# Kernel optimization log

Measured on AMD Instinct MI355X. Metric: run time of the kernel, lower is better.

Reference implementation:

```python
import jax, jax.numpy as jnp
import numpy as np

D_MODEL = 512; D_STATE = 64; D_CONV = 4; EXPAND = 1; HEADDIM = 128; NGROUPS = 2; CHUNK = 256
D_INNER = EXPAND * (D_MODEL // 2)          # 256
NHEADS = D_INNER // HEADDIM                 # 2
CONV_DIM = D_INNER + 2 * NGROUPS * D_STATE  # 512
D_IN_PROJ = CONV_DIM + NHEADS               # 514

def silu(x):
    return x * jax.nn.sigmoid(x)

def conv1x1(x, w, b):
    # x: (b,c,h,w), w: (o,c)
    return jnp.einsum('bchw,oc->bohw', x, w) + b[None, :, None, None]

def dwconv3x3(x, w, b):
    # depthwise 3x3, SAME padding; w: (c,1,3,3)
    c = x.shape[1]
    y = jax.lax.conv_general_dilated(x, w, (1, 1), 'SAME', feature_group_count=c,
                                     dimension_numbers=('NCHW', 'OIHW', 'NCHW'))
    return y + b[None, :, None, None]

def causal_dwconv1d(x, w, b):
    # x: (b,L,c); w: (c,k). Torch pads k-1 both sides then slices [:L] -> causal left pad.
    k = w.shape[1]
    xp = jnp.pad(x, ((0, 0), (k - 1, 0), (0, 0))).transpose(0, 2, 1)  # (b,c,L+k-1)
    y = jax.lax.conv_general_dilated(xp, w[:, None, :], (1,), 'VALID',
                                     feature_group_count=w.shape[0],
                                     dimension_numbers=('NCH', 'OIH', 'NCH'))
    return y.transpose(0, 2, 1) + b

def axis_attn(x, qw, qb, fw, fb, axis):
    # DualAxisAggAttn single-axis step
    qkv = conv1x1(x, qw, qb)
    c = x.shape[1]
    q, k, v = qkv[:, :1], qkv[:, 1:1 + c], qkv[:, 1 + c:]
    dim = -1 if axis == 'W' else -2
    scores = jax.nn.softmax(q, axis=dim)
    ctx = jnp.sum(k * scores, axis=dim, keepdims=True)
    out = x + jax.nn.sigmoid(v) * ctx
    return conv1x1(out, fw, fb)

def segsum(x):
    # x: (...,T) -> (...,T,T) lower-triangular segment sums, -inf above diagonal
    T = x.shape[-1]
    cs = jnp.cumsum(x, -1)
    d = cs[..., :, None] - cs[..., None, :]
    mask = jnp.tril(jnp.ones((T, T), bool))
    return jnp.where(mask, d, -jnp.inf)

def ssd(X, A, B, C, chunk):
    # Mamba2 SSD chunked scan. X: (b,l,h,p) = x*dt; A: (b,l,h) = dt*A_head; B,C: (b,l,h,n)
    b, l, h, p = X.shape; n = B.shape[-1]; c = l // chunk
    X = X.reshape(b, c, chunk, h, p)
    B = B.reshape(b, c, chunk, h, n)
    C = C.reshape(b, c, chunk, h, n)
    A = A.reshape(b, c, chunk, h).transpose(0, 3, 1, 2)  # (b,h,c,L)
    Acs = jnp.cumsum(A, -1)
    L = jnp.exp(segsum(A))  # (b,h,c,L,L) intra-chunk decay
    Yd = jnp.einsum('bclhn,bcshn,bhcls,bcshp->bclhp', C, B, L, X)
    dec = jnp.exp(Acs[..., -1:] - Acs)
    st = jnp.einsum('bclhn,bhcl,bclhp->bchpn', B, dec, X)  # chunk end-states
    st = jnp.concatenate([jnp.zeros_like(st[:, :1]), st], 1)
    dchunk = jnp.exp(segsum(jnp.pad(Acs[..., -1], ((0, 0), (0, 0), (1, 0)))))
    st = jnp.einsum('bhzc,bchpn->bzhpn', dchunk, st)[:, :-1]  # states entering each chunk
    Yo = jnp.einsum('bclhn,bchpn,bhcl->bclhp', C, st, jnp.exp(Acs))
    return (Yd + Yo).reshape(b, l, h, p)

def setup_inputs() -> dict:
    key = jax.random.key(0)
    ks = jax.random.split(key, 12)
    s = 0.02
    p = {}
    p['u'] = jax.random.normal(ks[0], (8, D_MODEL, 64, 64), jnp.float32)
    p['sc_w1'] = jax.random.normal(ks[1], (D_MODEL, D_MODEL)) * s
    p['sc_b1'] = jnp.zeros((D_MODEL,))
    p['sc_wdw'] = jax.random.normal(ks[2], (D_MODEL, 1, 3, 3)) * s
    p['sc_bdw'] = jnp.zeros((D_MODEL,))
    p['sc_w2'] = jax.random.normal(ks[3], (D_INNER, D_MODEL)) * s
    p['sc_b2'] = jnp.zeros((D_INNER,))
    p['mc_w'] = jax.random.normal(ks[4], (D_INNER, D_MODEL)) * s
    p['mc_b'] = jnp.zeros((D_INNER,))
    p['qkvW_w'] = jax.random.normal(ks[5], (1 + 2 * D_INNER, D_INNER)) * s
    p['qkvW_b'] = jnp.zeros((1 + 2 * D_INNER,))
    p['qkvH_w'] = jax.random.normal(ks[6], (1 + 2 * D_INNER, D_INNER)) * s
    p['qkvH_b'] = jnp.zeros((1 + 2 * D_INNER,))
    p['fuseW_w'] = jax.random.normal(ks[7], (D_INNER, D_INNER)) * s
    p['fuseW_b'] = jnp.zeros((D_INNER,))
    p['fuseH_w'] = jax.random.normal(ks[8], (D_INNER, D_INNER)) * s
    p['fuseH_b'] = jnp.zeros((D_INNER,))
    p['in_proj_w'] = jax.random.normal(ks[9], (D_IN_PROJ, D_INNER)) * s
    p['conv1d_w'] = jax.random.normal(ks[10], (CONV_DIM, D_CONV)) * s
    p['conv1d_b'] = jnp.zeros((CONV_DIM,))
    dt = np.exp(np.linspace(np.log(1e-3), np.log(0.1), NHEADS))
    p['dt_bias'] = jnp.asarray(dt + np.log(-np.expm1(-dt)), jnp.float32)
    p['A_log'] = jnp.asarray(np.log(np.linspace(1.0, 16.0, NHEADS)), jnp.float32)
    p['D'] = jnp.ones((NHEADS,))
    p['norm_w'] = jnp.ones((D_INNER,))
    p['outp_w'] = jax.random.normal(ks[11], (D_MODEL, 2 * D_INNER)) * s
    p['outp_b'] = jnp.zeros((D_MODEL,))
    return p

def reference(u, sc_w1, sc_b1, sc_wdw, sc_bdw, sc_w2, sc_b2, mc_w, mc_b,
              qkvW_w, qkvW_b, qkvH_w, qkvH_b, fuseW_w, fuseW_b, fuseH_w, fuseH_b,
              in_proj_w, conv1d_w, conv1d_b, dt_bias, A_log, D, norm_w, outp_w, outp_b):
    b, _, H, W = u.shape
    # short_conv branch (light_ConvBlock: 1x1 -> dw3x3 -> 1x1, all SiLU; BN folded into bias)
    z = silu(conv1x1(u, sc_w1, sc_b1))
    z = silu(dwconv3x3(z, sc_wdw, sc_bdw))
    z = silu(conv1x1(z, sc_w2, sc_b2))
    # main branch
    x = silu(conv1x1(u, mc_w, mc_b))
    x = axis_attn(x, qkvW_w, qkvW_b, fuseW_w, fuseW_b, 'W')
    x = axis_attn(x, qkvH_w, qkvH_b, fuseH_w, fuseH_b, 'H')
    seqlen = H * W
    u2 = x.transpose(0, 2, 3, 1).reshape(b, seqlen, D_INNER)  # b (h w) c
    xbcdt = u2 @ in_proj_w.T  # (b,l,d_in_proj)
    xBC = xbcdt[..., :CONV_DIM]
    dt = jax.nn.softplus(xbcdt[..., CONV_DIM:] + dt_bias)  # (b,l,h)
    A = -jnp.exp(A_log)  # (h,)
    xBC = silu(causal_dwconv1d(xBC, conv1d_w, conv1d_b))
    xs = xBC[..., :D_INNER]
    Bs = xBC[..., D_INNER:D_INNER + NGROUPS * D_STATE].reshape(b, seqlen, NGROUPS, D_STATE)
    Cs = xBC[..., D_INNER + NGROUPS * D_STATE:].reshape(b, seqlen, NGROUPS, D_STATE)
    Xh = xs.reshape(b, seqlen, NHEADS, HEADDIM)
    rep = NHEADS // NGROUPS
    Bh = jnp.repeat(Bs, rep, axis=2)
    Ch = jnp.repeat(Cs, rep, axis=2)
    y = ssd(Xh * dt[..., None], dt * A[None, None, :], Bh, Ch, CHUNK)
    y = y + Xh * D[None, None, :, None]  # D skip connection
    y = y.reshape(b, seqlen, D_INNER)
    # RMSNormGated with z=None -> plain RMSNorm
    y = y * jax.lax.rsqrt(jnp.mean(y * y, -1, keepdims=True) + 1e-5) * norm_w
    y = y.reshape(b, H, W, D_INNER).transpose(0, 3, 1, 2)
    y = jnp.concatenate([z, y], axis=1)
    return conv1x1(y, outp_w, outp_b)
```

## Files before the change

kernel.cpp:

```cpp
#include <hip/hip_runtime.h>
#include <hip/hip_bf16.h>
#include <cstddef>
#include <cstdint>

#define PTOT 32768
#define HWSZ 4096

typedef __attribute__((ext_vector_type(8))) short bf16x8;
typedef __attribute__((ext_vector_type(4))) short s16x4;
typedef __attribute__((ext_vector_type(4))) float f32x4;

__device__ __forceinline__ float sigf(float x){ return 1.f/(1.f+__expf(-x)); }
__device__ __forceinline__ float siluf(float x){ return x*sigf(x); }
__device__ __forceinline__ short f2b(float x){
  __hip_bfloat16 h = __float2bfloat16(x);
  return *reinterpret_cast<short*>(&h);
}
__device__ __forceinline__ float b2f(short s){
  unsigned u = ((unsigned)(unsigned short)s) << 16;
  return __uint_as_float(u);
}

__device__ __forceinline__ void gload16(const void* g, void* l){
  __builtin_amdgcn_global_load_lds(
      (const __attribute__((address_space(1))) unsigned int*)g,
      (__attribute__((address_space(3))) unsigned int*)l, 16, 0, 0);
}

__global__ __launch_bounds__(256) void k_cvtw(
    const float* __restrict__ s0, const float* __restrict__ s1, const float* __restrict__ s2,
    const float* __restrict__ s3, const float* __restrict__ s4, const float* __restrict__ s5,
    const float* __restrict__ s6, const float* __restrict__ s7, const float* __restrict__ s8,
    short* __restrict__ dst){
  int idx = blockIdx.x*256 + threadIdx.x;
  const float* s; int off;
  if      (idx <  262144){ s=s0; off=idx; }
  else if (idx <  393216){ s=s1; off=idx- 262144; }
  else if (idx <  524288){ s=s2; off=idx- 393216; }
  else if (idx <  655616){ s=s3; off=idx- 524288; }
  else if (idx <  786944){ s=s4; off=idx- 655616; }
  else if (idx <  852480){ s=s5; off=idx- 786944; }
  else if (idx <  918016){ s=s6; off=idx- 852480; }
  else if (idx < 1049600){ s=s7; off=idx- 918016; }
  else if (idx < 1311744){ s=s8; off=idx-1049600; }
  else return;
  dst[idx] = f2b(s[off]);
}

__global__ __launch_bounds__(256) void k_wcomp(
    const float* __restrict__ qkvHw, const float* __restrict__ fuWw,
    const float* __restrict__ fuWb,  const float* __restrict__ qkvHb,
    const float* __restrict__ inpw,  const float* __restrict__ fuHw,
    const float* __restrict__ fuHb,
    short* __restrict__ wcomb, float* __restrict__ bcomb,
    short* __restrict__ wi2,   float* __restrict__ bi2)
{
  int blk = blockIdx.x;
  int tid = threadIdx.x;
  __shared__ float as[256];
  __shared__ float red[256];
  if (blk < 513){
    int i = blk;
    int r = (i==512) ? 0 : (i+1);
    as[tid]  = qkvHw[(size_t)r*256 + tid];
    red[tid] = as[tid] * fuWb[tid];
    __syncthreads();
    for (int off=128; off; off>>=1){ if (tid<off) red[tid]+=red[tid+off]; __syncthreads(); }
    float acc = 0.f;
    #pragma unroll 8
    for (int k=0;k<256;k++) acc += as[k]*fuWw[(size_t)k*256 + tid];
    wcomb[(size_t)(256+i)*256 + tid] = f2b(acc);
    if (tid==0) bcomb[256+i] = red[0] + qkvHb[r];
  } else if (blk < 769){
    int j = blk - 513;
    wcomb[(size_t)j*256 + tid] = f2b(fuWw[(size_t)j*256 + tid]);
    if (tid==0) bcomb[j] = fuWb[j];
  } else {
    int j = blk - 769;
    as[tid]  = inpw[(size_t)j*256 + tid];
    red[tid] = as[tid] * fuHb[tid];
    __syncthreads();
    for (int off=128; off; off>>=1){ if (tid<off) red[tid]+=red[tid+off]; __syncthreads(); }
    float acc = 0.f;
    #pragma unroll 8
    for (int k=0;k<256;k++) acc += as[k]*fuHw[(size_t)k*256 + tid];
    wi2[(size_t)j*256 + tid] = f2b(acc);
    if (tid==0) bi2[j] = red[0];
  }
}

__global__ __launch_bounds__(256) void k_transpose(const float* __restrict__ in, short* __restrict__ out){
  __shared__ float tile[64][33];
  int b = blockIdx.z;
  int c0 = blockIdx.y * 64;
  int s0 = blockIdx.x * 32;
  int tx = threadIdx.x, ty = threadIdx.y;
  const float* ip = in + ((size_t)b*512 + c0)*HWSZ + s0;
  for (int i = ty; i < 64; i += 8) tile[i][tx] = ip[(size_t)i*HWSZ + tx];
  __syncthreads();
  for (int i = ty; i < 32; i += 8){
    unsigned lo = (unsigned)(unsigned short)f2b(tile[2*tx][i]);
    unsigned hi = (unsigned)(unsigned short)f2b(tile[2*tx+1][i]);
    unsigned pk = lo | (hi<<16);
    *reinterpret_cast<unsigned*>(&out[((size_t)((b<<12) + s0 + i))*512 + c0 + 2*tx]) = pk;
  }
}

template<int ACT, int OUT_NCHW>
__global__ __launch_bounds__(256) void k_gemm(
    const short* __restrict__ A0, const short* __restrict__ A1,
    int kSplit, int lda0, int lda1,
    const short* __restrict__ Wt, const float* __restrict__ bias,
    void* __restrict__ Cpv, int N, int K, int ldc, int qkvPerm)
{
  __shared__ short Alds[3][128*32];
  __shared__ short Blds[3][128*32];

  int tid = threadIdx.x;
  int lane = tid & 63;
  int wv = tid >> 6;
  int wr = wv >> 1, wc = wv & 1;
  int lr = lane & 15, lh = lane >> 4;
  int bm = blockIdx.x * 128;
  int bn = blockIdx.y * 128;

  int rl = lane >> 2;
  int kg = (lane & 3) << 3;

  int ar[2], wnr[2];
  #pragma unroll
  for (int j=0;j<2;j++){
    int r = wv*32 + j*16 + rl;
    ar[j] = bm + r;
    int n = bn + r; if (n > N-1) n = N-1;
    wnr[j] = qkvPerm ? ((n==512)?0:(n+1)) : n;
  }

  auto stage = [&](int buf, int t){
    int k0 = t << 5;
    #pragma unroll
    for (int j=0;j<2;j++){
      const short* asrc;
      if (k0 < kSplit) asrc = A0 + (size_t)ar[j]*lda0 + (k0 + kg);
      else             asrc = A1 + (size_t)ar[j]*lda1 + (k0 - kSplit + kg);
      gload16(asrc, &Alds[buf][(wv*32 + j*16)*32]);
      const short* bsrc = Wt + (size_t)wnr[j]*K + (k0 + kg);
      gload16(bsrc, &Blds[buf][(wv*32 + j*16)*32]);
    }
  };

  f32x4 acc[4][4];
  #pragma unroll
  for (int i=0;i<4;i++)
    #pragma unroll
    for (int j=0;j<4;j++) acc[i][j] = (f32x4){0.f,0.f,0.f,0.f};

  int NT = K >> 5;
  stage(0, 0);
  stage(1, 1);
  for (int t=0; t<NT; t++){
    int cur = t % 3;
    if (t+1 < NT) asm volatile("s_waitcnt vmcnt(4)" ::: "memory");
    else          asm volatile("s_waitcnt vmcnt(0)" ::: "memory");
    __builtin_amdgcn_s_barrier();
    __builtin_amdgcn_sched_barrier(0);
    if (t+2 < NT) stage((t+2)%3, t+2);
    bf16x8 af[4], bfr[4];
    #pragma unroll
    for (int mi=0;mi<4;mi++)
      af[mi] = *reinterpret_cast<const bf16x8*>(&Alds[cur][(wr*64 + mi*16 + lr)*32 + lh*8]);
    #pragma unroll
    for (int ni=0;ni<4;ni++)
      bfr[ni] = *reinterpret_cast<const bf16x8*>(&Blds[cur][(wc*64 + ni*16 + lr)*32 + lh*8]);
    #pragma unroll
    for (int mi=0;mi<4;mi++)
      #pragma unroll
      for (int ni=0;ni<4;ni++)
        acc[mi][ni] = __builtin_amdgcn_mfma_f32_16x16x32_bf16(af[mi], bfr[ni], acc[mi][ni], 0, 0, 0);
  }

  if (!OUT_NCHW){
    short* Cp = (short*)Cpv;
    #pragma unroll
    for (int mi=0;mi<4;mi++){
      int m = bm + wr*64 + mi*16 + lh*4;
      #pragma unroll
      for (int ni=0;ni<4;ni++){
        int n = bn + wc*64 + ni*16 + lr;
        if (n < N){
          int wn = qkvPerm ? ((n==512)?0:(n+1)) : n;
          float bb = bias ? bias[wn] : 0.f;
          #pragma unroll
          for (int r=0;r<4;r++){
            float v = acc[mi][ni][r] + bb;
            if (ACT==1) v = siluf(v);
            Cp[(size_t)(m+r)*ldc + n] = f2b(v);
          }
        }
      }
    }
  } else {
    float* Cp = (float*)Cpv;
    float* Sep = ((float*)Alds) + wv*16*68;
    #pragma unroll
    for (int mi=0;mi<4;mi++){
      __syncthreads();
      #pragma unroll
      for (int ni=0;ni<4;ni++){
        int n = bn + wc*64 + ni*16 + lr;
        float bb = (bias && n < N) ? bias[n] : 0.f;
        #pragma unroll
        for (int r=0;r<4;r++){
          float v = acc[mi][ni][r] + bb;
          if (ACT==1) v = siluf(v);
          Sep[(lh*4+r)*68 + ni*16 + lr] = v;
        }
      }
      __syncthreads();
      int m = bm + wr*64 + mi*16 + lr;
      size_t mb = ((size_t)(m>>12)*ldc)*HWSZ + (m & 4095);
      #pragma unroll
      for (int g=0; g<16; g++){
        int nl = g*4 + lh;
        float v = Sep[lr*68 + nl];
        int nn = bn + wc*64 + nl;
        if (nn < N) Cp[mb + (size_t)nn*HWSZ] = v;
      }
    }
  }
}

__global__ __launch_bounds__(256) void k_dwconv3x3(const short* __restrict__ in,
    const float* __restrict__ w, const float* __restrict__ bias, short* __restrict__ out){
  int tid = threadIdx.x;
  int cq = tid & 127;
  int wi = tid >> 7;
  int bw = blockIdx.x;
  int b  = bw >> 5;
  int wc = ((bw & 31) << 1) | wi;
  int h0 = blockIdx.y << 4;
  int c  = cq << 2;

  float arr[36];
  {
    const float* wp = &w[c*9];
    #pragma unroll
    for (int t=0;t<9;t++){
      f32x4 v = *reinterpret_cast<const f32x4*>(wp + t*4);
      arr[t*4+0]=v[0]; arr[t*4+1]=v[1]; arr[t*4+2]=v[2]; arr[t*4+3]=v[3];
    }
  }
  f32x4 bias4 = *reinterpret_cast<const f32x4*>(&bias[c]);

  int pb = b << 12;
  auto ldrow = [&](int r, int dw)->f32x4 {
    int ww = wc + dw;
    if ((unsigned)r >= 64u || (unsigned)ww >= 64u) return (f32x4){0.f,0.f,0.f,0.f};
    s16x4 v = *reinterpret_cast<const s16x4*>(&in[((size_t)(pb + (r<<6) + ww) << 9) + c]);
    return (f32x4){b2f(v[0]), b2f(v[1]), b2f(v[2]), b2f(v[3])};
  };

  f32x4 a00,a01,a02,a10,a11,a12,a20,a21,a22;
  a00=ldrow(h0-1,-1); a01=ldrow(h0-1,0); a02=ldrow(h0-1,1);
  a10=ldrow(h0  ,-1); a11=ldrow(h0  ,0); a12=ldrow(h0  ,1);
  #pragma unroll
  for (int hh=0; hh<16; hh++){
    int h = h0 + hh;
    a20=ldrow(h+1,-1); a21=ldrow(h+1,0); a22=ldrow(h+1,1);
    s16x4 o;
    #pragma unroll
    for (int j=0;j<4;j++){
      float v = bias4[j];
      v = fmaf(a00[j], arr[j*9+0], v);
      v = fmaf(a01[j], arr[j*9+1], v);
      v = fmaf(a02[j], arr[j*9+2], v);
      v = fmaf(a10[j], arr[j*9+3], v);
      v = fmaf(a11[j], arr[j*9+4], v);
      v = fmaf(a12[j], arr[j*9+5], v);
      v = fmaf(a20[j], arr[j*9+6], v);
      v = fmaf(a21[j], arr[j*9+7], v);
      v = fmaf(a22[j], arr[j*9+8], v);
      o[j] = f2b(siluf(v));
    }
    *reinterpret_cast<s16x4*>(&out[((size_t)(pb + (h<<6) + wc) << 9) + c]) = o;
    a00=a10; a01=a11; a02=a12;
    a10=a20; a11=a21; a12=a22;
  }
}

__global__ __launch_bounds__(256) void k_attn(const short* __restrict__ x, int xld,
    const short* __restrict__ qkv, int qld, short* __restrict__ out, int axisH){
  int bl = blockIdx.x;
  int b = bl >> 6, line = bl & 63;
  __shared__ float es[64];
  __shared__ float qs[64];
  int tid = threadIdx.x;
  int pbase = b << 12;
  if (tid < 64){
    int p = axisH ? (pbase | (tid<<6) | line) : (pbase | (line<<6) | tid);
    qs[tid] = b2f(qkv[(size_t)p*qld + 512]);
  }
  __syncthreads();
  float mx = -1e30f;
  for (int t=0;t<64;t++) mx = fmaxf(mx, qs[t]);
  if (tid < 64) es[tid] = __expf(qs[tid]-mx);
  __syncthreads();
  float s = 0.f;
  for (int t=0;t<64;t++) s += es[t];
  float inv = 1.f/s;
  int c = tid;
  float ctx = 0.f;
  for (int t=0;t<64;t++){
    int p = axisH ? (pbase | (t<<6) | line) : (pbase | (line<<6) | t);
    ctx += es[t]*b2f(qkv[(size_t)p*qld + c]);
  }
  ctx *= inv;
  for (int t=0;t<64;t++){
    int p = axisH ? (pbase | (t<<6) | line) : (pbase | (line<<6) | t);
    float vv = b2f(qkv[(size_t)p*qld + 256 + c]);
    float xv = b2f(x[(size_t)p*xld + c]);
    out[(size_t)p*256 + c] = f2b(xv + sigf(vv)*ctx);
  }
}

__global__ __launch_bounds__(256) void k_dt(const short* __restrict__ xbcdt,
    const float* __restrict__ dt_bias, float* __restrict__ dtb){
  int idx = blockIdx.x*256 + threadIdx.x;
  if (idx >= PTOT*2) return;
  int p = idx >> 1, h = idx & 1;
  float xv = b2f(xbcdt[(size_t)p*520 + 512 + h]) + dt_bias[h];
  float sp = (xv > 20.f) ? xv : log1pf(__expf(xv));
  dtb[idx] = sp;
}

__global__ __launch_bounds__(256) void k_conv1d(const short* __restrict__ xbcdt,
    const float* __restrict__ w, const float* __restrict__ bias, short* __restrict__ xBC){
  int tid = threadIdx.x;
  int cq = tid & 127;
  int c  = cq << 2;
  int half = tid >> 7;
  int bs = blockIdx.x;
  int b  = bs >> 7;
  int t0 = ((((bs & 127) << 1) | half) << 4);

  float wk[16];
  {
    const float* wp = &w[c*4];
    #pragma unroll
    for (int t=0;t<4;t++){
      f32x4 v = *reinterpret_cast<const f32x4*>(wp + t*4);
      wk[t*4+0]=v[0]; wk[t*4+1]=v[1]; wk[t*4+2]=v[2]; wk[t*4+3]=v[3];
    }
  }
  f32x4 bias4 = *reinterpret_cast<const f32x4*>(&bias[c]);

  int pb = b << 12;
  auto ld = [&](int t)->f32x4 {
    if (t < 0) return (f32x4){0.f,0.f,0.f,0.f};
    s16x4 v = *reinterpret_cast<const s16x4*>(&xbcdt[(size_t)(pb + t)*520 + c]);
    return (f32x4){b2f(v[0]), b2f(v[1]), b2f(v[2]), b2f(v[3])};
  };

  f32x4 x0,x1,x2,x3;
  x0 = ld(t0-3); x1 = ld(t0-2); x2 = ld(t0-1);
  #pragma unroll
  for (int tt=0; tt<16; tt++){
    int t = t0 + tt;
    x3 = ld(t);
    s16x4 o;
    #pragma unroll
    for (int j=0;j<4;j++){
      float v = bias4[j];
      v = fmaf(x0[j], wk[j*4+0], v);
      v = fmaf(x1[j], wk[j*4+1], v);
      v = fmaf(x2[j], wk[j*4+2], v);
      v = fmaf(x3[j], wk[j*4+3], v);
      o[j] = f2b(siluf(v));
    }
    *reinterpret_cast<s16x4*>(&xBC[((size_t)(pb + t) << 9) + c]) = o;
    x0=x1; x1=x2; x2=x3;
  }
}

__global__ __launch_bounds__(256) void k_ssd_states(
  const short* __restrict__ xBC, const float* __restrict__ dtb, const float* __restrict__ A_log,
  float* __restrict__ states, float* __restrict__ AcsG, float* __restrict__ AtotG)
{
  int ci = blockIdx.x, h = blockIdx.y, b = blockIdx.z;
  int tid = threadIdx.x;
  __shared__ float sa[256], sb[256];
  __shared__ float Bs[64][65];
  __shared__ float Xs[64][136];
  int base = (b<<12) | (ci<<8);
  float Ah = -__expf(A_log[h]);
  sa[tid] = dtb[(size_t)(base + tid)*2 + h] * Ah;
  __syncthreads();
  float* src = sa; float* dst = sb;
  for (int off=1; off<256; off<<=1){
    float v = src[tid];
    if (tid >= off) v += src[tid - off];
    dst[tid] = v;
    __syncthreads();
    float* tswap = src; src = dst; dst = tswap;
  }
  float acs = src[tid];
  float atot = src[255];
  AcsG[((size_t)((b*2+h)*16 + ci))*256 + tid] = acs;
  if (tid == 0) AtotG[(b*2+h)*16 + ci] = atot;

  int tn = tid >> 4;
  int tp = tid & 15;
  float acc[4][8];
  #pragma unroll
  for (int i=0;i<4;i++)
    #pragma unroll
    for (int j=0;j<8;j++) acc[i][j]=0.f;

  for (int t0=0; t0<256; t0+=64){
    __syncthreads();
    for (int e = tid; e < 64*64; e += 256){
      int t = e >> 6, n = e & 63;
      float d = __expf(atot - src[t0 + t]);
      Bs[t][n] = b2f(xBC[(size_t)(base + t0 + t)*512 + 256 + (h<<6) + n]) * d;
    }
    for (int e = tid; e < 64*128; e += 256){
      int t = e >> 7, pp = e & 127;
      Xs[t][pp] = b2f(xBC[(size_t)(base + t0 + t)*512 + (h<<7) + pp]) * dtb[(size_t)(base + t0 + t)*2 + h];
    }
    __syncthreads();
    for (int t=0;t<64;t++){
      float bv[4], xv[8];
      #pragma unroll
      for (int i=0;i<4;i++) bv[i]=Bs[t][tn*4+i];
      #pragma unroll
      for (int j=0;j<8;j++) xv[j]=Xs[t][tp*8+j];
      #pragma unroll
      for (int i=0;i<4;i++)
        #pragma unroll
        for (int j=0;j<8;j++) acc[i][j] = fmaf(bv[i], xv[j], acc[i][j]);
    }
  }
  float* stp = states + (((size_t)(b*16+ci)*2 + h) << 13);
  #pragma unroll
  for (int i=0;i<4;i++){
    float4 s0 = {acc[i][0], acc[i][1], acc[i][2], acc[i][3]};
    float4 s1 = {acc[i][4], acc[i][5], acc[i][6], acc[i][7]};
    float* pdst = &stp[(tn*4+i)*128 + tp*8];
    *reinterpret_cast<float4*>(pdst)   = s0;
    *reinterpret_cast<float4*>(pdst+4) = s1;
  }
}

__global__ __launch_bounds__(256) void k_ssd_scan(const float* __restrict__ states,
    const float* __restrict__ AtotG, float* __restrict__ R){
  int bh = blockIdx.x;
  int b = bh >> 1, h = bh & 1;
  int tid = threadIdx.x;
  float r[32];
  #pragma unroll
  for (int j=0;j<32;j++) r[j]=0.f;
  for (int ci=0; ci<16; ci++){
    size_t off = (((size_t)(b*16+ci)*2) + h) << 13;
    #pragma unroll
    for (int j=0;j<32;j++) R[off + tid + (j<<8)] = r[j];
    if (ci < 15){
      float sc = __expf(AtotG[bh*16 + ci]);
      #pragma unroll
      for (int j=0;j<32;j++) r[j] = fmaf(sc, r[j], states[off + tid + (j<<8)]);
    }
  }
}

__global__ __launch_bounds__(256) void k_ssd_y(
  const short* __restrict__ xBC, const float* __restrict__ dtb,
  const float* __restrict__ AcsG, const float* __restrict__ R,
  const float* __restrict__ Dp, float* __restrict__ yraw)
{
  int bx = blockIdx.x;
  int ci = bx >> 2, lt = bx & 3;
  int h = blockIdx.y, b = blockIdx.z;
  int tid = threadIdx.x, lane = tid & 63, w = tid >> 6;
  int lg = lane >> 4, lr = lane & 15;
  int base = (b<<12) | (ci<<8);
  int l0 = lt << 6;

  __shared__ short Cbf[64*72];
  __shared__ short Bbf[64*72];
  __shared__ short Xt [128*76];
  __shared__ short Sbf[64*72];
  __shared__ float acs_l[64], acs_s[64], dt_s[64];

  const float* acsrow = AcsG + ((size_t)((b*2+h)*16 + ci))*256;

  {
    int row = tid >> 2, c0 = (tid & 3) << 4;
    const short* src = &xBC[(size_t)(base + l0 + row)*512 + 384 + (h<<6) + c0];
    *reinterpret_cast<bf16x8*>(&Cbf[row*72 + c0])     = *reinterpret_cast<const bf16x8*>(src);
    *reinterpret_cast<bf16x8*>(&Cbf[row*72 + c0 + 8]) = *reinterpret_cast<const bf16x8*>(src+8);
  }
  if (tid < 64) acs_l[tid] = acsrow[l0 + tid];

  f32x4 yacc[8];
  #pragma unroll
  for (int pf=0;pf<8;pf++) yacc[pf] = (f32x4){0.f,0.f,0.f,0.f};

  for (int s0 = 0; s0 <= l0; s0 += 64){
    __syncthreads();
    {
      int row = tid >> 2, c0 = (tid & 3) << 4;
      const short* src = &xBC[(size_t)(base + s0 + row)*512 + 256 + (h<<6) + c0];
      *reinterpret_cast<bf16x8*>(&Bbf[row*72 + c0])     = *reinterpret_cast<const bf16x8*>(src);
      *reinterpret_cast<bf16x8*>(&Bbf[row*72 + c0 + 8]) = *reinterpret_cast<const bf16x8*>(src+8);
    }
    {
      int s = tid >> 2;
      int p0 = (tid & 3) << 5;
      const short* src = &xBC[(size_t)(base + s0 + s)*512 + (h<<7) + p0];
      #pragma unroll
      for (int q=0;q<4;q++){
        bf16x8 v = *reinterpret_cast<const bf16x8*>(src + q*8);
        #pragma unroll
        for (int e=0;e<8;e++) Xt[(p0 + q*8 + e)*76 + s] = v[e];
      }
    }
    if (tid < 64){
      acs_s[tid] = acsrow[s0 + tid];
      dt_s[tid]  = dtb[(size_t)(base + s0 + tid)*2 + h];
    }
    __syncthreads();

    f32x4 sacc[4];
    #pragma unroll
    for (int f=0;f<4;f++) sacc[f] = (f32x4){0.f,0.f,0.f,0.f};
    bf16x8 ca0 = *reinterpret_cast<const bf16x8*>(&Cbf[(w*16+lr)*72 + lg*8]);
    bf16x8 ca1 = *reinterpret_cast<const bf16x8*>(&Cbf[(w*16+lr)*72 + 32 + lg*8]);
    #pragma unroll
    for (int f=0;f<4;f++){
      bf16x8 bb0 = *reinterpret_cast<const bf16x8*>(&Bbf[(f*16+lr)*72 + lg*8]);
      bf16x8 bb1 = *reinterpret_cast<const bf16x8*>(&Bbf[(f*16+lr)*72 + 32 + lg*8]);
      sacc[f] = __builtin_amdgcn_mfma_f32_16x16x32_bf16(ca0, bb0, sacc[f], 0, 0, 0);
      sacc[f] = __builtin_amdgcn_mfma_f32_16x16x32_bf16(ca1, bb1, sacc[f], 0, 0, 0);
    }
    #pragma unroll
    for (int f=0;f<4;f++){
      #pragma unroll
      for (int r=0;r<4;r++){
        int ll = w*16 + lg*4 + r;
        int ss = f*16 + lr;
        float v = 0.f;
        if (s0 + ss <= l0 + ll)
          v = sacc[f][r] * __expf(acs_l[ll] - acs_s[ss]) * dt_s[ss];
        Sbf[ll*72 + ss] = f2b(v);
      }
    }
    __syncthreads();

    bf16x8 sa0 = *reinterpret_cast<const bf16x8*>(&Sbf[(w*16+lr)*72 + lg*8]);
    bf16x8 sa1 = *reinterpret_cast<const bf16x8*>(&Sbf[(w*16+lr)*72 + 32 + lg*8]);
    #pragma unroll
    for (int pf=0;pf<8;pf++){
      bf16x8 x0 = *reinterpret_cast<const bf16x8*>(&Xt[(pf*16+lr)*76 + lg*8]);
      bf16x8 x1 = *reinterpret_cast<const bf16x8*>(&Xt[(pf*16+lr)*76 + 32 + lg*8]);
      yacc[pf] = __builtin_amdgcn_mfma_f32_16x16x32_bf16(sa0, x0, yacc[pf], 0, 0, 0);
      yacc[pf] = __builtin_amdgcn_mfma_f32_16x16x32_bf16(sa1, x1, yacc[pf], 0, 0, 0);
    }
  }

  __syncthreads();
  {
    size_t roff = (((size_t)(b*16+ci)*2) + h) << 13;
    int n = tid >> 2;
    const float* src = R + roff + (size_t)n*128;
    #pragma unroll
    for (int j=0;j<8;j++){
      int p = ((tid & 3) << 2) + (j << 4);
      float4 f = *reinterpret_cast<const float4*>(&src[p]);
      Xt[(p+0)*76 + n] = f2b(f.x);
      Xt[(p+1)*76 + n] = f2b(f.y);
      Xt[(p+2)*76 + n] = f2b(f.z);
      Xt[(p+3)*76 + n] = f2b(f.w);
    }
  }
  __syncthreads();
  f32x4 racc[8];
  #pragma unroll
  for (int pf=0;pf<8;pf++) racc[pf] = (f32x4){0.f,0.f,0.f,0.f};
  {
    bf16x8 ca0 = *reinterpret_cast<const bf16x8*>(&Cbf[(w*16+lr)*72 + lg*8]);
    bf16x8 ca1 = *reinterpret_cast<const bf16x8*>(&Cbf[(w*16+lr)*72 + 32 + lg*8]);
    #pragma unroll
    for (int pf=0;pf<8;pf++){
      bf16x8 x0 = *reinterpret_cast<const bf16x8*>(&Xt[(pf*16+lr)*76 + lg*8]);
      bf16x8 x1 = *reinterpret_cast<const bf16x8*>(&Xt[(pf*16+lr)*76 + 32 + lg*8]);
      racc[pf] = __builtin_amdgcn_mfma_f32_16x16x32_bf16(ca0, x0, racc[pf], 0, 0, 0);
      racc[pf] = __builtin_amdgcn_mfma_f32_16x16x32_bf16(ca1, x1, racc[pf], 0, 0, 0);
    }
  }

  float Dh = Dp[h];
  float el[4];
  #pragma unroll
  for (int r=0;r<4;r++) el[r] = __expf(acs_l[w*16 + lg*4 + r]);
  #pragma unroll
  for (int pf=0;pf<8;pf++){
    #pragma unroll
    for (int r=0;r<4;r++){
      int ll = w*16 + lg*4 + r;
      int p = pf*16 + lr;
      size_t pix = (size_t)(base + l0 + ll);
      float xraw = b2f(xBC[pix*512 + (h<<7) + p]);
      yraw[pix*256 + (h<<7) + p] = yacc[pf][r] + el[r]*racc[pf][r] + Dh*xraw;
    }
  }
}

__global__ __launch_bounds__(256) void k_rmsnorm(const float* __restrict__ yraw,
    const float* __restrict__ nw, short* __restrict__ ynorm){
  int p = blockIdx.x;
  int tid = threadIdx.x;
  float v = yraw[(size_t)p*256 + tid];
  float sq = v*v;
  for (int off=32; off; off>>=1) sq += __shfl_down(sq, off);
  __shared__ float wsum[4];
  if ((tid & 63) == 0) wsum[tid>>6] = sq;
  __syncthreads();
  float tot = wsum[0]+wsum[1]+wsum[2]+wsum[3];
  float scale = rsqrtf(tot*(1.f/256.f) + 1e-5f);
  ynorm[(size_t)p*256 + tid] = f2b(v*scale*nw[tid]);
}

extern "C" void kernel_launch(void* const* d_in, const int* in_sizes, int n_in,
                              void* d_out, int out_size, void* d_ws, size_t ws_size,
                              hipStream_t stream)
{
  (void)in_sizes; (void)n_in; (void)out_size; (void)ws_size;
  const float* u        = (const float*)d_in[0];
  const float* sc_w1    = (const float*)d_in[1];
  const float* sc_b1    = (const float*)d_in[2];
  const float* sc_wdw   = (const float*)d_in[3];
  const float* sc_bdw   = (const float*)d_in[4];
  const float* sc_w2    = (const float*)d_in[5];
  const float* sc_b2    = (const float*)d_in[6];
  const float* mc_w     = (const float*)d_in[7];
  const float* mc_b     = (const float*)d_in[8];
  const float* qkvW_w   = (const float*)d_in[9];
  const float* qkvW_b   = (const float*)d_in[10];
  const float* qkvH_w   = (const float*)d_in[11];
  const float* qkvH_b   = (const float*)d_in[12];
  const float* fuseW_w  = (const float*)d_in[13];
  const float* fuseW_b  = (const float*)d_in[14];
  const float* fuseH_w  = (const float*)d_in[15];
  const float* fuseH_b  = (const float*)d_in[16];
  const float* in_proj_w= (const float*)d_in[17];
  const float* conv1d_w = (const float*)d_in[18];
  const float* conv1d_b = (const float*)d_in[19];
  const float* dt_bias  = (const float*)d_in[20];
  const float* A_log    = (const float*)d_in[21];
  const float* Dp       = (const float*)d_in[22];
  const float* norm_w   = (const float*)d_in[23];
  const float* outp_w   = (const float*)d_in[24];
  const float* outp_b   = (const float*)d_in[25];

  char* wsb = (char*)d_ws;
  size_t off = 0;
  auto alloc = [&](size_t bytes){ void* p = wsb + off; off = (off + bytes + 255) & ~(size_t)255; return p; };
  short* wbf   = (short*)alloc((size_t)1640192*2);
  float* bcomb = (float*)alloc(769*4);
  float* bi2   = (float*)alloc(514*4);
  short* slotB = (short*)alloc((size_t)PTOT*776*2);
  short* slotC = (short*)alloc((size_t)PTOT*512*2);
  short* slotZ = (short*)alloc((size_t)PTOT*256*2);
  short* slotE = (short*)alloc((size_t)PTOT*256*2);
  float* slotF = (float*)alloc((size_t)PTOT*256*4);
  float* slotS = (float*)alloc((size_t)4460000*4);

  float* dtb     = slotS;
  float* AcsG    = slotS + 65536;
  float* AtotG   = slotS + 131072;
  float* statesB = slotS + 131328;
  float* Rb      = slotS + 131328 + 2097152;
  short* ynorm   = slotE;
  short* xwh     = (short*)slotF;

  short* w_sc1  = wbf + 0;
  short* w_sc2  = wbf + 262144;
  short* w_mc   = wbf + 393216;
  short* w_qkvW = wbf + 524288;
  short* w_outp = wbf + 1049600;
  short* wcomb  = wbf + 1311744;
  short* wi2    = wbf + 1311744 + 196864;

  short* u_pm = (short*)d_out;
  float* out  = (float*)d_out;

  const int BIG = 1<<30;

  k_cvtw<<<5124, 256, 0, stream>>>(sc_w1, sc_w2, mc_w, qkvW_w, qkvH_w, fuseW_w, fuseH_w, in_proj_w, outp_w, wbf);
  k_wcomp<<<1283, 256, 0, stream>>>(qkvH_w, fuseW_w, fuseW_b, qkvH_b, in_proj_w, fuseH_w, fuseH_b,
                                    wcomb, bcomb, wi2, bi2);
  k_transpose<<<dim3(128,8,8), dim3(32,8), 0, stream>>>(u, u_pm);

  k_gemm<1,0><<<dim3(256,4), 256, 0, stream>>>(u_pm, u_pm, BIG, 512, 512, w_sc1, sc_b1, slotB, 512, 512, 512, 0);
  k_dwconv3x3<<<dim3(256,4), 256, 0, stream>>>(slotB, sc_wdw, sc_bdw, slotC);
  k_gemm<1,0><<<dim3(256,2), 256, 0, stream>>>(slotC, slotC, BIG, 512, 512, w_sc2, sc_b2, slotZ, 256, 512, 256, 0);

  k_gemm<1,0><<<dim3(256,2), 256, 0, stream>>>(u_pm, u_pm, BIG, 512, 512, w_mc, mc_b, slotE, 256, 512, 256, 0);
  k_gemm<0,0><<<dim3(256,5), 256, 0, stream>>>(slotE, slotE, BIG, 256, 256, w_qkvW, qkvW_b, slotB, 513, 256, 520, 1);
  k_attn<<<512, 256, 0, stream>>>(slotE, 256, slotB, 520, xwh, 0);
  k_gemm<0,0><<<dim3(256,7), 256, 0, stream>>>(xwh, xwh, BIG, 256, 256, wcomb, bcomb, slotB, 769, 256, 776, 0);
  k_attn<<<512, 256, 0, stream>>>(slotB, 776, slotB + 256, 776, xwh, 1);
  k_gemm<0,0><<<dim3(256,5), 256, 0, stream>>>(xwh, xwh, BIG, 256, 256, wi2, bi2, slotB, 514, 256, 520, 0);
  k_dt<<<256, 256, 0, stream>>>(slotB, dt_bias, dtb);
  k_conv1d<<<1024, 256, 0, stream>>>(slotB, conv1d_w, conv1d_b, slotC);

  k_ssd_states<<<dim3(16,2,8), 256, 0, stream>>>(slotC, dtb, A_log, statesB, AcsG, AtotG);
  k_ssd_scan<<<16, 256, 0, stream>>>(statesB, AtotG, Rb);
  k_ssd_y<<<dim3(64,2,8), 256, 0, stream>>>(slotC, dtb, AcsG, Rb, Dp, slotF);

  k_rmsnorm<<<32768, 256, 0, stream>>>(slotF, norm_w, ynorm);

  k_gemm<0,1><<<dim3(256,4), 256, 0, stream>>>(slotZ, ynorm, 256, 256, 256, w_outp, outp_b, out, 512, 512, 512, 0);
}
```

Measured before the change: 485.2 us.

## Fuse shortcut and main-branch input GEMMs and trim weight conversion

The sc1 and mc 1x1 convolutions share the same input, so their weights are concatenated and run as one 768-wide GEMM, with outputs split across two buffers in the epilogue. This removes a separate launch and a second read of the input activation. Weight conversion now skips the qkvH, fuse and in_proj matrices, which were never used directly since only the precomputed combined weights are read. The GEMM pipeline also changes to double-buffered weight tiles with a lower vmcnt wait threshold and sched barriers; this adds a per-element branch in the epilogue and changes load ordering.

```diff
diff --git a/kernel.cpp b/kernel.cpp
--- a/kernel.cpp
+++ b/kernel.cpp
@@ -29,8 +29,7 @@
 
 __global__ __launch_bounds__(256) void k_cvtw(
     const float* __restrict__ s0, const float* __restrict__ s1, const float* __restrict__ s2,
-    const float* __restrict__ s3, const float* __restrict__ s4, const float* __restrict__ s5,
-    const float* __restrict__ s6, const float* __restrict__ s7, const float* __restrict__ s8,
+    const float* __restrict__ s3, const float* __restrict__ s4,
     short* __restrict__ dst){
   int idx = blockIdx.x*256 + threadIdx.x;
   const float* s; int off;
@@ -38,11 +37,7 @@
   else if (idx <  393216){ s=s1; off=idx- 262144; }
   else if (idx <  524288){ s=s2; off=idx- 393216; }
   else if (idx <  655616){ s=s3; off=idx- 524288; }
-  else if (idx <  786944){ s=s4; off=idx- 655616; }
-  else if (idx <  852480){ s=s5; off=idx- 786944; }
-  else if (idx <  918016){ s=s6; off=idx- 852480; }
-  else if (idx < 1049600){ s=s7; off=idx- 918016; }
-  else if (idx < 1311744){ s=s8; off=idx-1049600; }
+  else if (idx <  917760){ s=s4; off=idx- 655616; }
   else return;
   dst[idx] = f2b(s[off]);
 }
@@ -52,8 +47,10 @@
     const float* __restrict__ fuWb,  const float* __restrict__ qkvHb,
     const float* __restrict__ inpw,  const float* __restrict__ fuHw,
     const float* __restrict__ fuHb,
+    const float* __restrict__ scb1,  const float* __restrict__ mcb,
     short* __restrict__ wcomb, float* __restrict__ bcomb,
-    short* __restrict__ wi2,   float* __restrict__ bi2)
+    short* __restrict__ wi2,   float* __restrict__ bi2,
+    float* __restrict__ bzx)
 {
   int blk = blockIdx.x;
   int tid = threadIdx.x;
@@ -75,7 +72,7 @@
     int j = blk - 513;
     wcomb[(size_t)j*256 + tid] = f2b(fuWw[(size_t)j*256 + tid]);
     if (tid==0) bcomb[j] = fuWb[j];
-  } else {
+  } else if (blk < 1283){
     int j = blk - 769;
     as[tid]  = inpw[(size_t)j*256 + tid];
     red[tid] = as[tid] * fuHb[tid];
@@ -86,6 +83,9 @@
     for (int k=0;k<256;k++) acc += as[k]*fuHw[(size_t)k*256 + tid];
     wi2[(size_t)j*256 + tid] = f2b(acc);
     if (tid==0) bi2[j] = red[0];
+  } else {
+    int j = (blk - 1283)*256 + tid;
+    bzx[j] = (j < 512) ? scb1[j] : mcb[j-512];
   }
 }
 
@@ -111,10 +111,11 @@
     const short* __restrict__ A0, const short* __restrict__ A1,
     int kSplit, int lda0, int lda1,
     const short* __restrict__ Wt, const float* __restrict__ bias,
-    void* __restrict__ Cpv, int N, int K, int ldc, int qkvPerm)
+    void* __restrict__ Cpv, int N, int K, int ldc, int qkvPerm,
+    short* __restrict__ Cp2, int nSplit2, int ldc2)
 {
   __shared__ short Alds[3][128*32];
-  __shared__ short Blds[3][128*32];
+  __shared__ short Wlds[2][128*32];
 
   int tid = threadIdx.x;
   int lane = tid & 63;
@@ -136,7 +137,7 @@
     wnr[j] = qkvPerm ? ((n==512)?0:(n+1)) : n;
   }
 
-  auto stage = [&](int buf, int t){
+  auto stage_a = [&](int buf, int t){
     int k0 = t << 5;
     #pragma unroll
     for (int j=0;j<2;j++){
@@ -144,8 +145,14 @@
       if (k0 < kSplit) asrc = A0 + (size_t)ar[j]*lda0 + (k0 + kg);
       else             asrc = A1 + (size_t)ar[j]*lda1 + (k0 - kSplit + kg);
       gload16(asrc, &Alds[buf][(wv*32 + j*16)*32]);
+    }
+  };
+  auto stage_w = [&](int buf, int t){
+    int k0 = t << 5;
+    #pragma unroll
+    for (int j=0;j<2;j++){
       const short* bsrc = Wt + (size_t)wnr[j]*K + (k0 + kg);
-      gload16(bsrc, &Blds[buf][(wv*32 + j*16)*32]);
+      gload16(bsrc, &Wlds[buf][(wv*32 + j*16)*32]);
     }
   };
 
@@ -156,22 +163,28 @@
     for (int j=0;j<4;j++) acc[i][j] = (f32x4){0.f,0.f,0.f,0.f};
 
   int NT = K >> 5;
-  stage(0, 0);
-  stage(1, 1);
+  stage_w(0, 0);
+  __builtin_amdgcn_sched_barrier(0);
+  stage_a(0, 0);
+  __builtin_amdgcn_sched_barrier(0);
+  stage_a(1, 1);
   for (int t=0; t<NT; t++){
-    int cur = t % 3;
-    if (t+1 < NT) asm volatile("s_waitcnt vmcnt(4)" ::: "memory");
+    int ab = t % 3, wb = t & 1;
+    if (t+1 < NT) asm volatile("s_waitcnt vmcnt(2)" ::: "memory");
     else          asm volatile("s_waitcnt vmcnt(0)" ::: "memory");
     __builtin_amdgcn_s_barrier();
     __builtin_amdgcn_sched_barrier(0);
-    if (t+2 < NT) stage((t+2)%3, t+2);
+    if (t+1 < NT) stage_w(wb^1, t+1);
+    __builtin_amdgcn_sched_barrier(0);
+    if (t+2 < NT) stage_a((t+2)%3, t+2);
+    __builtin_amdgcn_sched_barrier(0);
     bf16x8 af[4], bfr[4];
     #pragma unroll
     for (int mi=0;mi<4;mi++)
-      af[mi] = *reinterpret_cast<const bf16x8*>(&Alds[cur][(wr*64 + mi*16 + lr)*32 + lh*8]);
+      af[mi] = *reinterpret_cast<const bf16x8*>(&Alds[ab][(wr*64 + mi*16 + lr)*32 + lh*8]);
     #pragma unroll
     for (int ni=0;ni<4;ni++)
-      bfr[ni] = *reinterpret_cast<const bf16x8*>(&Blds[cur][(wc*64 + ni*16 + lr)*32 + lh*8]);
+      bfr[ni] = *reinterpret_cast<const bf16x8*>(&Wlds[wb][(wc*64 + ni*16 + lr)*32 + lh*8]);
     #pragma unroll
     for (int mi=0;mi<4;mi++)
       #pragma unroll
@@ -194,7 +207,9 @@
           for (int r=0;r<4;r++){
             float v = acc[mi][ni][r] + bb;
             if (ACT==1) v = siluf(v);
-            Cp[(size_t)(m+r)*ldc + n] = f2b(v);
+            short sv = f2b(v);
+            if (n < nSplit2) Cp[(size_t)(m+r)*ldc + n] = sv;
+            else             Cp2[(size_t)(m+r)*ldc2 + (n - nSplit2)] = sv;
           }
         }
       }
@@ -664,9 +679,10 @@
   char* wsb = (char*)d_ws;
   size_t off = 0;
   auto alloc = [&](size_t bytes){ void* p = wsb + off; off = (off + bytes + 255) & ~(size_t)255; return p; };
-  short* wbf   = (short*)alloc((size_t)1640192*2);
+  short* wbf   = (short*)alloc((size_t)1246208*2);
   float* bcomb = (float*)alloc(769*4);
   float* bi2   = (float*)alloc(514*4);
+  float* bzx   = (float*)alloc(768*4);
   short* slotB = (short*)alloc((size_t)PTOT*776*2);
   short* slotC = (short*)alloc((size_t)PTOT*512*2);
   short* slotZ = (short*)alloc((size_t)PTOT*256*2);
@@ -682,34 +698,37 @@
   short* ynorm   = slotE;
   short* xwh     = (short*)slotF;
 
-  short* w_sc1  = wbf + 0;
-  short* w_sc2  = wbf + 262144;
-  short* w_mc   = wbf + 393216;
+  short* w_zx   = wbf + 0;
+  short* w_sc2  = wbf + 393216;
   short* w_qkvW = wbf + 524288;
-  short* w_outp = wbf + 1049600;
-  short* wcomb  = wbf + 1311744;
-  short* wi2    = wbf + 1311744 + 196864;
+  short* w_outp = wbf + 655616;
+  short* wcomb  = wbf + 917760;
+  short* wi2    = wbf + 1114624;
 
   short* u_pm = (short*)d_out;
   float* out  = (float*)d_out;
 
   const int BIG = 1<<30;
 
-  k_cvtw<<<5124, 256, 0, stream>>>(sc_w1, sc_w2, mc_w, qkvW_w, qkvH_w, fuseW_w, fuseH_w, in_proj_w, outp_w, wbf);
-  k_wcomp<<<1283, 256, 0, stream>>>(qkvH_w, fuseW_w, fuseW_b, qkvH_b, in_proj_w, fuseH_w, fuseH_b,
-                                    wcomb, bcomb, wi2, bi2);
+  k_cvtw<<<3585, 256, 0, stream>>>(sc_w1, mc_w, sc_w2, qkvW_w, outp_w, wbf);
+  k_wcomp<<<1286, 256, 0, stream>>>(qkvH_w, fuseW_w, fuseW_b, qkvH_b, in_proj_w, fuseH_w, fuseH_b,
+                                    sc_b1, mc_b, wcomb, bcomb, wi2, bi2, bzx);
   k_transpose<<<dim3(128,8,8), dim3(32,8), 0, stream>>>(u, u_pm);
 
-  k_gemm<1,0><<<dim3(256,4), 256, 0, stream>>>(u_pm, u_pm, BIG, 512, 512, w_sc1, sc_b1, slotB, 512, 512, 512, 0);
+  k_gemm<1,0><<<dim3(256,6), 256, 0, stream>>>(u_pm, u_pm, BIG, 512, 512, w_zx, bzx,
+                                               slotB, 768, 512, 512, 0, slotE, 512, 256);
   k_dwconv3x3<<<dim3(256,4), 256, 0, stream>>>(slotB, sc_wdw, sc_bdw, slotC);
-  k_gemm<1,0><<<dim3(256,2), 256, 0, stream>>>(slotC, slotC, BIG, 512, 512, w_sc2, sc_b2, slotZ, 256, 512, 256, 0);
-
-  k_gemm<1,0><<<dim3(256,2), 256, 0, stream>>>(u_pm, u_pm, BIG, 512, 512, w_mc, mc_b, slotE, 256, 512, 256, 0);
-  k_gemm<0,0><<<dim3(256,5), 256, 0, stream>>>(slotE, slotE, BIG, 256, 256, w_qkvW, qkvW_b, slotB, 513, 256, 520, 1);
+  k_gemm<1,0><<<dim3(256,2), 256, 0, stream>>>(slotC, slotC, BIG, 512, 512, w_sc2, sc_b2,
+                                               slotZ, 256, 512, 256, 0, nullptr, BIG, 0);
+
+  k_gemm<0,0><<<dim3(256,5), 256, 0, stream>>>(slotE, slotE, BIG, 256, 256, w_qkvW, qkvW_b,
+                                               slotB, 513, 256, 520, 1, nullptr, BIG, 0);
   k_attn<<<512, 256, 0, stream>>>(slotE, 256, slotB, 520, xwh, 0);
-  k_gemm<0,0><<<dim3(256,7), 256, 0, stream>>>(xwh, xwh, BIG, 256, 256, wcomb, bcomb, slotB, 769, 256, 776, 0);
+  k_gemm<0,0><<<dim3(256,7), 256, 0, stream>>>(xwh, xwh, BIG, 256, 256, wcomb, bcomb,
+                                               slotB, 769, 256, 776, 0, nullptr, BIG, 0);
   k_attn<<<512, 256, 0, stream>>>(slotB, 776, slotB + 256, 776, xwh, 1);
-  k_gemm<0,0><<<dim3(256,5), 256, 0, stream>>>(xwh, xwh, BIG, 256, 256, wi2, bi2, slotB, 514, 256, 520, 0);
+  k_gemm<0,0><<<dim3(256,5), 256, 0, stream>>>(xwh, xwh, BIG, 256, 256, wi2, bi2,
+                                               slotB, 514, 256, 520, 0, nullptr, BIG, 0);
   k_dt<<<256, 256, 0, stream>>>(slotB, dt_bias, dtb);
   k_conv1d<<<1024, 256, 0, stream>>>(slotB, conv1d_w, conv1d_b, slotC);
 
@@ -719,5 +738,6 @@
 
   k_rmsnorm<<<32768, 256, 0, stream>>>(slotF, norm_w, ynorm);
 
-  k_gemm<0,1><<<dim3(256,4), 256, 0, stream>>>(slotZ, ynorm, 256, 256, 256, w_outp, outp_b, out, 512, 512, 512, 0);
-}
+  k_gemm<0,1><<<dim3(256,4), 256, 0, stream>>>(slotZ, ynorm, 256, 256, 256, w_outp, outp_b,
+                                               out, 512, 512, 512, 0, nullptr, BIG, 0);
+}
```

Result: no change. 477.3 us (-1.6%).
